# Kernel optimization log

Measured on AMD Instinct MI355X. Metric: run time of the kernel, lower is better.

## Reference

```python
import jax, jax.numpy as jnp
import numpy as np

B, L, DIM, H = 2, 2048, 2048, 16
D = DIM // H
EPS = 1e-6
CAP = 50.0
SCALE = D ** -0.5


def _rms_norm(x, w):
    # x: [B,H,L,D], normalize over last dim
    scale = jax.lax.rsqrt(jnp.maximum(jnp.mean(x * x, axis=-1, keepdims=True), EPS))
    return w * x * scale


def _rotate_half(x):
    x1, x2 = jnp.split(x, 2, axis=-1)
    return jnp.concatenate([-x2, x1], axis=-1)


def setup_inputs() -> dict:
    key = jax.random.key(0)
    ks = jax.random.split(key, 6)
    x = jax.random.normal(ks[0], (B, L, DIM), dtype=jnp.float32)
    w_qkv = jax.random.normal(ks[1], (3 * DIM, DIM), dtype=jnp.float32) * (DIM ** -0.5)
    w_out = jax.random.normal(ks[2], (DIM, DIM), dtype=jnp.float32) * (DIM ** -0.5)
    q_norm_w = jnp.ones((D,), dtype=jnp.float32)
    k_norm_w = jnp.ones((D,), dtype=jnp.float32)
    # rope tables [L, D]
    inv_freq = 1.0 / (10000.0 ** (np.arange(0, D, 2, dtype=np.float32) / D))
    t = np.arange(L, dtype=np.float32)
    freqs = np.outer(t, inv_freq)  # [L, D/2]
    emb = np.concatenate([freqs, freqs], axis=-1)  # [L, D]
    cos = jnp.asarray(np.cos(emb), dtype=jnp.float32)
    sin = jnp.asarray(np.sin(emb), dtype=jnp.float32)
    # additive causal mask [1,1,L,L]
    causal = np.triu(np.full((L, L), -1e9, dtype=np.float32), k=1)
    mask = jnp.asarray(causal)[None, None]
    return {"x": x, "w_qkv": w_qkv, "w_out": w_out, "q_norm_w": q_norm_w,
            "k_norm_w": k_norm_w, "cos": cos, "sin": sin, "mask": mask}


def reference(x, w_qkv, w_out, q_norm_w, k_norm_w, cos, sin, mask):
    b, l, _ = x.shape
    qkv = jnp.einsum('bld,ed->ble', x, w_qkv).reshape(b, l, 3, H, D)
    q, k, v = [jnp.transpose(qkv[:, :, i], (0, 2, 1, 3)) for i in range(3)]  # [B,H,L,D]
    q = _rms_norm(q, q_norm_w)
    k = _rms_norm(k, k_norm_w)
    # rope: cos/sin are [L,D] -> [1,1,L,D]
    c = cos[-l:, :][None, None]
    s = sin[-l:, :][None, None]
    q = q * c + _rotate_half(q) * s
    k = k * c + _rotate_half(k) * s
    attn = jnp.einsum('bhqd,bhkd->bhqk', q, k) * SCALE
    attn = jnp.tanh(attn / CAP) * CAP + mask
    probs = jax.nn.softmax(attn, axis=-1)
    o = jnp.einsum('bhqk,bhkd->bhqd', probs, v)
    o = jnp.transpose(o, (0, 2, 1, 3)).reshape(b, l, H * D)
    out = jnp.einsum('bld,ed->ble', o, w_out)
    return (out, (k, v))
```

## Files before the change

kernel.cpp:

```cpp
#include <hip/hip_runtime.h>
#include <hip/hip_bf16.h>
#include <stdint.h>

#define LL 2048
#define DD 128
#define HH 16

typedef float f32x4 __attribute__((ext_vector_type(4)));
typedef float f32x2 __attribute__((ext_vector_type(2)));
typedef short bf16x8 __attribute__((ext_vector_type(8)));
typedef short short4v __attribute__((ext_vector_type(4)));
typedef float float4v __attribute__((ext_vector_type(4)));

__device__ __forceinline__ float bf2f(short s) {
  union { unsigned u; float f; } v; v.u = ((unsigned)(unsigned short)s) << 16; return v.f;
}
__device__ __forceinline__ short f2bf(float f) {
  union { float f; unsigned u; } v; v.f = f;
  unsigned u = v.u;
  u += 0x7fffu + ((u >> 16) & 1u);
  return (short)(u >> 16);
}

__device__ __forceinline__ void gload_lds16(const void* g, void* lds) {
  __builtin_amdgcn_global_load_lds(
      (__attribute__((address_space(1))) unsigned int*)(void*)(uintptr_t)g,
      (__attribute__((address_space(3))) unsigned int*)lds, 16, 0, 0);
}

__global__ __launch_bounds__(256) void cast_all_kernel(
    const float* __restrict__ x, const float* __restrict__ wqkv,
    const float* __restrict__ wout, short* __restrict__ dst)
{
  long i4 = ((long)blockIdx.x * 256 + threadIdx.x) * 4;
  const float* src; long off;
  if (i4 < 8388608L)        { src = x;    off = i4; }
  else if (i4 < 20971520L)  { src = wqkv; off = i4 - 8388608L; }
  else                      { src = wout; off = i4 - 20971520L; }
  float4v v = *(const float4v*)(src + off);
  short4v o;
  o.x = f2bf(v.x); o.y = f2bf(v.y); o.z = f2bf(v.z); o.w = f2bf(v.w);
  *(short4v*)(dst + i4) = o;
}

template <typename OutT>
__global__ __launch_bounds__(256) void gemm_bt_kernel(
    const short* __restrict__ A, const short* __restrict__ Bm,
    OutT* __restrict__ C, int M, int N, int K)
{
  __shared__ __align__(16) short As[128 * 64];
  __shared__ __align__(16) short Bs[128 * 64];
  const int tid = threadIdx.x;
  const int lane = tid & 63;
  const int g = lane >> 4, j = lane & 15;
  const int m0 = blockIdx.y * 128, n0 = blockIdx.x * 128;
  const int wave = tid >> 6;
  const int wm = (wave >> 1) * 64, wn = (wave & 1) * 64;

  f32x4 acc[4][4];
  const f32x4 z = {0.f, 0.f, 0.f, 0.f};
#pragma unroll
  for (int i = 0; i < 4; ++i)
#pragma unroll
    for (int jj = 0; jj < 4; ++jj) acc[i][jj] = z;

  for (int k0 = 0; k0 < K; k0 += 64) {
#pragma unroll
    for (int it = 0; it < 4; ++it) {
      int c = it * 256 + tid;
      int row = c >> 3, ko = (c & 7) << 3;
      gload_lds16(A + (size_t)(m0 + row) * K + k0 + ko, As + c * 8);
    }
#pragma unroll
    for (int it = 0; it < 4; ++it) {
      int c = it * 256 + tid;
      int row = c >> 3, ko = (c & 7) << 3;
      gload_lds16(Bm + (size_t)(n0 + row) * K + k0 + ko, Bs + c * 8);
    }
    __syncthreads();
#pragma unroll
    for (int ks = 0; ks < 2; ++ks) {
      bf16x8 af[4], bfr[4];
#pragma unroll
      for (int i = 0; i < 4; ++i)
        af[i] = *(const bf16x8*)(As + (wm + i * 16 + j) * 64 + ks * 32 + g * 8);
#pragma unroll
      for (int i = 0; i < 4; ++i)
        bfr[i] = *(const bf16x8*)(Bs + (wn + i * 16 + j) * 64 + ks * 32 + g * 8);
#pragma unroll
      for (int i = 0; i < 4; ++i)
#pragma unroll
        for (int jj = 0; jj < 4; ++jj)
          acc[i][jj] = __builtin_amdgcn_mfma_f32_16x16x32_bf16(af[i], bfr[jj], acc[i][jj], 0, 0, 0);
    }
    __syncthreads();
  }
#pragma unroll
  for (int i = 0; i < 4; ++i)
#pragma unroll
    for (int jj = 0; jj < 4; ++jj)
#pragma unroll
      for (int r = 0; r < 4; ++r) {
        int row = m0 + wm + i * 16 + g * 4 + r;
        int col = n0 + wn + jj * 16 + j;
        if constexpr (sizeof(OutT) == 4)
          C[(size_t)row * N + col] = acc[i][jj][r];
        else
          C[(size_t)row * N + col] = f2bf(acc[i][jj][r]);
      }
}

__global__ __launch_bounds__(256) void normrope_kernel(
    const short* __restrict__ qkv, const float* __restrict__ qw,
    const float* __restrict__ kw, const float* __restrict__ cosb,
    const float* __restrict__ sinb, short* __restrict__ qo,
    float* __restrict__ ko, short* __restrict__ kb, float* __restrict__ vo)
{
  int wid = (blockIdx.x * 256 + threadIdx.x) >> 6;
  int lane = threadIdx.x & 63;
  int h = wid & 15;
  int rest = wid >> 4;
  int t = rest % 3;
  int bl = rest / 3;
  int l = bl & (LL - 1);
  int d0 = lane * 2;
  const short* src = qkv + (size_t)bl * 6144 + t * 2048 + h * 128 + d0;
  int raw = *(const int*)src;
  float v0 = bf2f((short)(raw & 0xffff));
  float v1 = bf2f((short)((raw >> 16) & 0xffff));
  size_t oidx = ((size_t)((bl >> 11) * HH + h) * LL + l) * DD + d0;
  if (t == 2) {
    f32x2 vv = {v0, v1};
    *(f32x2*)(vo + oidx) = vv;
    return;
  }
  float ss = v0 * v0 + v1 * v1;
#pragma unroll
  for (int m = 1; m <= 32; m <<= 1) ss += __shfl_xor(ss, m, 64);
  float scale = rsqrtf(fmaxf(ss * (1.0f / 128.0f), 1e-6f));
  const float* w = (t == 0) ? qw : kw;
  float n0 = w[d0] * v0 * scale;
  float n1 = w[d0 + 1] * v1 * scale;
  float c0 = cosb[l * 128 + d0], c1 = cosb[l * 128 + d0 + 1];
  float s0 = sinb[l * 128 + d0], s1 = sinb[l * 128 + d0 + 1];
  float p0 = __shfl_xor(n0, 32, 64);
  float p1 = __shfl_xor(n1, 32, 64);
  float r0 = (lane < 32) ? -p0 : p0;
  float r1 = (lane < 32) ? -p1 : p1;
  float o0 = n0 * c0 + r0 * s0;
  float o1 = n1 * c1 + r1 * s1;
  int pk = (int)((unsigned short)f2bf(o0) | ((unsigned)(unsigned short)f2bf(o1) << 16));
  if (t == 0) {
    *(int*)(qo + oidx) = pk;
  } else {
    f32x2 kk = {o0, o1};
    *(f32x2*)(ko + oidx) = kk;
    *(int*)(kb + oidx) = pk;
  }
}

__global__ __launch_bounds__(256) void transpose_v_kernel(
    const float* __restrict__ v, short* __restrict__ vT)
{
  __shared__ __align__(16) short tl[64 * 72];
  int bid = blockIdx.x;
  int dt = bid & 1;
  int lt = (bid >> 1) & 31;
  int bh = bid >> 6;
  int tid = threadIdx.x;
#pragma unroll
  for (int it = 0; it < 4; ++it) {
    int c = it * 256 + tid;
    int row = c >> 4, off = (c & 15) << 2;
    float4v val = *(const float4v*)(v + ((size_t)bh * LL + lt * 64 + row) * DD + dt * 64 + off);
    short4v s;
    s.x = f2bf(val.x); s.y = f2bf(val.y); s.z = f2bf(val.z); s.w = f2bf(val.w);
    *(short4v*)(tl + row * 72 + off) = s;
  }
  __syncthreads();
#pragma unroll
  for (int it = 0; it < 2; ++it) {
    int c = it * 256 + tid;
    int dr = c >> 3, lo = (c & 7) << 3;
    bf16x8 o;
#pragma unroll
    for (int i = 0; i < 8; ++i) o[i] = tl[(lo + i) * 72 + dr];
    *(bf16x8*)(vT + ((size_t)bh * DD + dt * 64 + dr) * LL + lt * 64 + lo) = o;
  }
}

__global__ __launch_bounds__(256, 2) void attn_kernel(
    const short* __restrict__ q, const short* __restrict__ k,
    const short* __restrict__ vT, short* __restrict__ o)
{
  __shared__ __align__(16) short Ks[64 * 136];
  __shared__ __align__(16) short Vs[128 * 72];
  __shared__ __align__(16) short Ps[128 * 72];
  int bid = blockIdx.x;
  int bh = bid & 31;
  int gq = (bid >> 5) & 7;
  int qt = (bid < 256) ? (15 - gq) : gq;
  int b = bh >> 4;
  int h = bh & 15;
  int tid = threadIdx.x;
  int lane = tid & 63;
  int w = tid >> 6;
  int g = lane >> 4, j = lane & 15;
  int q0 = qt * 128;
  int wrow = q0 + w * 32;

  bf16x8 qf[2][4];
#pragma unroll
  for (int mi = 0; mi < 2; ++mi)
#pragma unroll
    for (int ks = 0; ks < 4; ++ks)
      qf[mi][ks] = *(const bf16x8*)(q + ((size_t)bh * LL + wrow + mi * 16 + j) * DD + ks * 32 + g * 8);

  f32x4 accO[2][8];
  const f32x4 z = {0.f, 0.f, 0.f, 0.f};
#pragma unroll
  for (int mi = 0; mi < 2; ++mi)
#pragma unroll
    for (int n = 0; n < 8; ++n) accO[mi][n] = z;
  float lsum[2][4] = {{0.f,0.f,0.f,0.f},{0.f,0.f,0.f,0.f}};

  const float c2 = 0.0035355339059327379f;
  int ktmax = 2 * qt + 1;
  for (int kt = 0; kt <= ktmax; ++kt) {
    int k0 = kt * 64;
#pragma unroll
    for (int it = 0; it < 4; ++it) {
      int c = it * 256 + tid;
      int row = c >> 4, off = (c & 15) << 3;
      bf16x8 val = *(const bf16x8*)(k + ((size_t)bh * LL + k0 + row) * DD + off);
      *(bf16x8*)(Ks + row * 136 + off) = val;
    }
#pragma unroll
    for (int it = 0; it < 4; ++it) {
      int c = it * 256 + tid;
      int row = c >> 3, off = (c & 7) << 3;
      bf16x8 val = *(const bf16x8*)(vT + ((size_t)bh * DD + row) * LL + k0 + off);
      *(bf16x8*)(Vs + row * 72 + off) = val;
    }
    __syncthreads();

    f32x4 sa[2][4];
#pragma unroll
    for (int mi = 0; mi < 2; ++mi)
#pragma unroll
      for (int n = 0; n < 4; ++n) sa[mi][n] = z;
#pragma unroll
    for (int ks = 0; ks < 4; ++ks) {
#pragma unroll
      for (int n = 0; n < 4; ++n) {
        bf16x8 kf = *(const bf16x8*)(Ks + (n * 16 + j) * 136 + ks * 32 + g * 8);
#pragma unroll
        for (int mi = 0; mi < 2; ++mi)
          sa[mi][n] = __builtin_amdgcn_mfma_f32_16x16x32_bf16(qf[mi][ks], kf, sa[mi][n], 0, 0, 0);
      }
    }

#pragma unroll
    for (int mi = 0; mi < 2; ++mi) {
      const bool wmask = (k0 + 63) > (wrow + mi * 16);
#pragma unroll
      for (int r = 0; r < 4; ++r) {
        int row_g = wrow + mi * 16 + g * 4 + r;
#pragma unroll
        for (int n = 0; n < 4; ++n) {
          float e2 = __expf(sa[mi][n][r] * c2);
          float t = 38.f - 100.f * __builtin_amdgcn_rcpf(e2 + 1.f);
          float p = __expf(t);
          if (wmask && (k0 + n * 16 + j > row_g)) p = 0.f;
          lsum[mi][r] += p;
          Ps[(w * 32 + mi * 16 + g * 4 + r) * 72 + n * 16 + j] = f2bf(p);
        }
      }
    }
#pragma unroll
    for (int ks = 0; ks < 2; ++ks) {
      bf16x8 pf[2];
#pragma unroll
      for (int mi = 0; mi < 2; ++mi)
        pf[mi] = *(const bf16x8*)(Ps + (w * 32 + mi * 16 + j) * 72 + ks * 32 + g * 8);
#pragma unroll
      for (int n = 0; n < 8; ++n) {
        bf16x8 vf = *(const bf16x8*)(Vs + (n * 16 + j) * 72 + ks * 32 + g * 8);
#pragma unroll
        for (int mi = 0; mi < 2; ++mi)
          accO[mi][n] = __builtin_amdgcn_mfma_f32_16x16x32_bf16(pf[mi], vf, accO[mi][n], 0, 0, 0);
      }
    }
    __syncthreads();
  }

#pragma unroll
  for (int mi = 0; mi < 2; ++mi)
#pragma unroll
    for (int r = 0; r < 4; ++r) {
#pragma unroll
      for (int m = 1; m <= 8; m <<= 1) lsum[mi][r] += __shfl_xor(lsum[mi][r], m, 64);
    }

#pragma unroll
  for (int mi = 0; mi < 2; ++mi) {
    size_t obase = ((size_t)b * LL + wrow + mi * 16) * 2048 + h * 128;
#pragma unroll
    for (int r = 0; r < 4; ++r) {
      float inv = 1.f / lsum[mi][r];
#pragma unroll
      for (int n = 0; n < 8; ++n)
        o[obase + (size_t)(g * 4 + r) * 2048 + n * 16 + j] = f2bf(accO[mi][n][r] * inv);
    }
  }
}

extern "C" void kernel_launch(void* const* d_in, const int* in_sizes, int n_in,
                              void* d_out, int out_size, void* d_ws, size_t ws_size,
                              hipStream_t stream) {
  const float* x    = (const float*)d_in[0];
  const float* wqkv = (const float*)d_in[1];
  const float* wout = (const float*)d_in[2];
  const float* qw   = (const float*)d_in[3];
  const float* kw   = (const float*)d_in[4];
  const float* cosb = (const float*)d_in[5];
  const float* sinb = (const float*)d_in[6];

  float* out   = (float*)d_out;
  float* k_out = out + 8388608;
  float* v_out = out + 16777216;

  short* ws    = (short*)d_ws;
  short* xb    = ws;
  short* wqkvb = ws + 8388608;
  short* woutb = ws + 20971520;
  short* qkv   = ws + 25165824;
  short* qbuf  = xb;
  short* kbuf  = wqkvb;
  short* vT    = qkv;
  short* obuf  = qkv + 8388608;

  cast_all_kernel<<<24576, 256, 0, stream>>>(x, wqkv, wout, ws);
  gemm_bt_kernel<short><<<dim3(48, 32), 256, 0, stream>>>(xb, wqkvb, qkv, 4096, 6144, 2048);
  normrope_kernel<<<49152, 256, 0, stream>>>(qkv, qw, kw, cosb, sinb, qbuf, k_out, kbuf, v_out);
  transpose_v_kernel<<<2048, 256, 0, stream>>>(v_out, vT);
  attn_kernel<<<512, 256, 0, stream>>>(qbuf, kbuf, vT, obuf);
  gemm_bt_kernel<float><<<dim3(16, 32), 256, 0, stream>>>(obuf, woutb, out, 4096, 2048, 2048);
}
```

Before: 351.0 us.

## Replace QKV projection GEMM with 256x256 tile, 8-wave pipelined kernel

Adds a new GEMM for the QKV projection with 256x256 output tiles, 512 threads, and double-buffered LDS. Global loads go straight to LDS through global_load_lds with an XOR swizzle, and stages are interleaved with MFMA quarters under explicit barriers, vmcnt waits and setprio. The larger tile raises arithmetic intensity per LDS/global byte and overlaps loads with compute. The cost is more LDS (128KB), higher register pressure and a hand-scheduled pipeline with many barriers.

```diff
diff --git a/kernel.cpp b/kernel.cpp
--- a/kernel.cpp
+++ b/kernel.cpp
@@ -41,6 +41,126 @@
   short4v o;
   o.x = f2bf(v.x); o.y = f2bf(v.y); o.z = f2bf(v.z); o.w = f2bf(v.w);
   *(short4v*)(dst + i4) = o;
+}
+
+#define SCHED __builtin_amdgcn_sched_barrier(0)
+#define BARRIER { SCHED; __builtin_amdgcn_s_barrier(); SCHED; }
+
+#define STAGE(buf, opx, ptr, rb, ks, t)                                        \
+  { _Pragma("unroll") for (int l_ = 0; l_ < 2; ++l_) {                          \
+      int ch_ = l_ * 512 + tid;                                                 \
+      int row_ = ch_ >> 2, ci_ = ch_ & 3;                                       \
+      gload_lds16(ptr + (size_t)(rb + row_) * K + (t) * 64 + (ks) * 32 +        \
+                      ((ci_ ^ (row_ & 3)) << 3),                                \
+                  &lds[buf][opx][ks][ch_ << 3]);                                \
+  } }
+
+#define LDA(buf, mh, ks)                                                       \
+  { _Pragma("unroll") for (int mf_ = 0; mf_ < 4; ++mf_) {                       \
+      int r_ = wm * 128 + (mh) * 64 + mf_ * 16 + j;                             \
+      areg[mf_] = *(const bf16x8*)&lds[buf][0][ks][r_ * 32 + ((g ^ (j & 3)) << 3)]; \
+  } }
+
+#define LDB(dst, buf, ks)                                                      \
+  { _Pragma("unroll") for (int nf_ = 0; nf_ < 4; ++nf_) {                       \
+      int r_ = wn * 64 + nf_ * 16 + j;                                          \
+      dst[nf_] = *(const bf16x8*)&lds[buf][1][ks][r_ * 32 + ((g ^ (j & 3)) << 3)]; \
+  } }
+
+#define MFMAQ(mh, breg)                                                        \
+  { __builtin_amdgcn_s_setprio(1);                                             \
+    _Pragma("unroll") for (int mf_ = 0; mf_ < 4; ++mf_)                         \
+      _Pragma("unroll") for (int nf_ = 0; nf_ < 4; ++nf_)                       \
+        acc[(mh) * 4 + mf_][nf_] = __builtin_amdgcn_mfma_f32_16x16x32_bf16(     \
+            areg[mf_], breg[nf_], acc[(mh) * 4 + mf_][nf_], 0, 0, 0);           \
+    __builtin_amdgcn_s_setprio(0); }
+
+__global__ __launch_bounds__(512, 2) void gemm256_kernel(
+    const short* __restrict__ A, const short* __restrict__ Bm,
+    short* __restrict__ C, int M, int N, int K)
+{
+  __shared__ __align__(16) short lds[2][2][2][8192];
+  const int tid = threadIdx.x;
+  const int lane = tid & 63;
+  const int wid = tid >> 6;
+  const int wm = wid >> 2, wn = wid & 3;
+  const int g = lane >> 4, j = lane & 15;
+  const int m0 = blockIdx.y * 256, n0 = blockIdx.x * 256;
+  const int NT = K >> 6;
+
+  f32x4 acc[8][4];
+  const f32x4 z = {0.f, 0.f, 0.f, 0.f};
+#pragma unroll
+  for (int im = 0; im < 8; ++im)
+#pragma unroll
+    for (int nf = 0; nf < 4; ++nf) acc[im][nf] = z;
+
+  STAGE(0, 1, Bm, n0, 0, 0); STAGE(0, 1, Bm, n0, 1, 0);
+  STAGE(0, 0, A,  m0, 0, 0); STAGE(0, 0, A,  m0, 1, 0);
+  STAGE(1, 1, Bm, n0, 0, 1); STAGE(1, 1, Bm, n0, 1, 1);
+  STAGE(1, 0, A,  m0, 0, 1);
+  asm volatile("s_waitcnt vmcnt(6)" ::: "memory");
+  __builtin_amdgcn_s_barrier();
+  SCHED;
+
+  bf16x8 areg[4], b0r[4], b1r[4];
+#pragma unroll 1
+  for (int i = 0; i < (NT >> 1) - 1; ++i) {
+    int t0 = i * 2;
+    LDA(0, 0, 0); LDB(b0r, 0, 0);
+    STAGE(1, 0, A, m0, 1, t0 + 1);
+    BARRIER; MFMAQ(0, b0r); BARRIER;
+    LDA(0, 0, 1); LDB(b1r, 0, 1);
+    STAGE(0, 1, Bm, n0, 0, t0 + 2);
+    BARRIER; MFMAQ(0, b1r); BARRIER;
+    LDA(0, 1, 0);
+    STAGE(0, 1, Bm, n0, 1, t0 + 2);
+    BARRIER; MFMAQ(1, b0r); BARRIER;
+    LDA(0, 1, 1);
+    STAGE(0, 0, A, m0, 0, t0 + 2);
+    BARRIER; MFMAQ(1, b1r);
+    SCHED; asm volatile("s_waitcnt vmcnt(6)" ::: "memory");
+    __builtin_amdgcn_s_barrier(); SCHED;
+    LDA(1, 0, 0); LDB(b0r, 1, 0);
+    STAGE(0, 0, A, m0, 1, t0 + 2);
+    BARRIER; MFMAQ(0, b0r); BARRIER;
+    LDA(1, 0, 1); LDB(b1r, 1, 1);
+    STAGE(1, 1, Bm, n0, 0, t0 + 3);
+    BARRIER; MFMAQ(0, b1r); BARRIER;
+    LDA(1, 1, 0);
+    STAGE(1, 1, Bm, n0, 1, t0 + 3);
+    BARRIER; MFMAQ(1, b0r); BARRIER;
+    LDA(1, 1, 1);
+    STAGE(1, 0, A, m0, 0, t0 + 3);
+    BARRIER; MFMAQ(1, b1r);
+    SCHED; asm volatile("s_waitcnt vmcnt(6)" ::: "memory");
+    __builtin_amdgcn_s_barrier(); SCHED;
+  }
+  {
+    LDA(0, 0, 0); LDB(b0r, 0, 0);
+    STAGE(1, 0, A, m0, 1, NT - 1);
+    BARRIER; MFMAQ(0, b0r); BARRIER;
+    LDA(0, 0, 1); LDB(b1r, 0, 1);
+    BARRIER; MFMAQ(0, b1r); BARRIER;
+    LDA(0, 1, 0);
+    BARRIER; MFMAQ(1, b0r); BARRIER;
+    LDA(0, 1, 1);
+    BARRIER; MFMAQ(1, b1r);
+    SCHED; asm volatile("s_waitcnt vmcnt(0)" ::: "memory");
+    __builtin_amdgcn_s_barrier(); SCHED;
+    LDA(1, 0, 0); LDB(b0r, 1, 0); MFMAQ(0, b0r);
+    LDA(1, 0, 1); LDB(b1r, 1, 1); MFMAQ(0, b1r);
+    LDA(1, 1, 0); MFMAQ(1, b0r);
+    LDA(1, 1, 1); MFMAQ(1, b1r);
+  }
+#pragma unroll
+  for (int im = 0; im < 8; ++im)
+#pragma unroll
+    for (int nf = 0; nf < 4; ++nf)
+#pragma unroll
+      for (int r = 0; r < 4; ++r)
+        C[(size_t)(m0 + wm * 128 + im * 16 + g * 4 + r) * N + n0 + wn * 64 + nf * 16 + j] =
+            f2bf(acc[im][nf][r]);
 }
 
 template <typename OutT>
@@ -341,7 +461,7 @@
   short* obuf  = qkv + 8388608;
 
   cast_all_kernel<<<24576, 256, 0, stream>>>(x, wqkv, wout, ws);
-  gemm_bt_kernel<short><<<dim3(48, 32), 256, 0, stream>>>(xb, wqkvb, qkv, 4096, 6144, 2048);
+  gemm256_kernel<<<dim3(24, 16), 512, 0, stream>>>(xb, wqkvb, qkv, 4096, 6144, 2048);
   normrope_kernel<<<49152, 256, 0, stream>>>(qkv, qw, kw, cosb, sinb, qbuf, k_out, kbuf, v_out);
   transpose_v_kernel<<<2048, 256, 0, stream>>>(v_out, vT);
   attn_kernel<<<512, 256, 0, stream>>>(qbuf, kbuf, vT, obuf);
```

Result: faster. 320.8 us (-8.6%).

## Replace QKV projection GEMM with 256x256 double-buffered pipelined MFMA kernel

Applied to the files above, without the earlier changes.

Adds a new 512-thread GEMM kernel that computes 256x256 output tiles and is used for the QKV projection. It double-buffers LDS with direct global-to-LDS loads, uses XOR-swizzled LDS layouts, and interleaves LDS fragment reads with MFMA issue under explicit waitcnt, barrier and priority control. The aim is more data reuse per tile and better overlap of memory and compute than the old 128x128 kernel. The loop hardcodes K=2048 (32 k-tiles) and tile-multiple dimensions, and the larger register and LDS footprint may limit occupancy.

```diff
diff --git a/kernel.cpp b/kernel.cpp
--- a/kernel.cpp
+++ b/kernel.cpp
@@ -41,6 +41,111 @@
   short4v o;
   o.x = f2bf(v.x); o.y = f2bf(v.y); o.z = f2bf(v.z); o.w = f2bf(v.w);
   *(short4v*)(dst + i4) = o;
+}
+
+#define SCHED __builtin_amdgcn_sched_barrier(0)
+#define BARRIER { SCHED; __builtin_amdgcn_s_barrier(); SCHED; }
+#define LGKM(n) { asm volatile("s_waitcnt lgkmcnt(" #n ")" ::: "memory"); SCHED; }
+#define VMC(n)  { asm volatile("s_waitcnt vmcnt(" #n ")" ::: "memory"); SCHED; }
+
+#define STAGE(buf, opx, ptr, rb, ks, t)                                        \
+  { _Pragma("unroll") for (int l_ = 0; l_ < 2; ++l_) {                          \
+      int ch_ = l_ * 512 + tid;                                                 \
+      int row_ = ch_ >> 2, ci_ = ch_ & 3;                                       \
+      gload_lds16(ptr + (size_t)(rb + row_) * K + (t) * 64 + (ks) * 32 +        \
+                      ((ci_ ^ ((row_ >> 1) & 3)) << 3),                         \
+                  &lds[buf][opx][ks][ch_ << 3]);                                \
+  } }
+
+#define STAGE_TILE(buf, t)                                                     \
+  { STAGE(buf, 0, A,  m0, 0, t); STAGE(buf, 0, A,  m0, 1, t);                   \
+    STAGE(buf, 1, Bm, n0, 0, t); STAGE(buf, 1, Bm, n0, 1, t); }
+
+#define LDA_TO(dst, buf, mh)                                                   \
+  { _Pragma("unroll") for (int ks_ = 0; ks_ < 2; ++ks_)                         \
+    _Pragma("unroll") for (int mf_ = 0; mf_ < 4; ++mf_) {                       \
+      int r_ = wm * 128 + (mh) * 64 + mf_ * 16 + j;                             \
+      dst[ks_][mf_] = *(const bf16x8*)&lds[buf][0][ks_][r_ * 32 + ((g ^ ((j >> 1) & 3)) << 3)]; \
+  } }
+
+#define LDB_TO(dst, buf)                                                       \
+  { _Pragma("unroll") for (int ks_ = 0; ks_ < 2; ++ks_)                         \
+    _Pragma("unroll") for (int nf_ = 0; nf_ < 4; ++nf_) {                       \
+      int r_ = wn * 64 + nf_ * 16 + j;                                          \
+      dst[ks_][nf_] = *(const bf16x8*)&lds[buf][1][ks_][r_ * 32 + ((g ^ ((j >> 1) & 3)) << 3)]; \
+  } }
+
+#define MFMA32(asrc, mh)                                                       \
+  { __builtin_amdgcn_s_setprio(1);                                             \
+    _Pragma("unroll") for (int ks_ = 0; ks_ < 2; ++ks_)                         \
+      _Pragma("unroll") for (int mf_ = 0; mf_ < 4; ++mf_)                       \
+        _Pragma("unroll") for (int nf_ = 0; nf_ < 4; ++nf_)                     \
+          acc[(mh) * 4 + mf_][nf_] = __builtin_amdgcn_mfma_f32_16x16x32_bf16(   \
+              asrc[ks_][mf_], bb[ks_][nf_], acc[(mh) * 4 + mf_][nf_], 0, 0, 0); \
+    __builtin_amdgcn_s_setprio(0); }
+
+#define TILE_BODY(B, t, DO_STAGE, DO_PF, VKIND)                                \
+  {                                                                            \
+    LDB_TO(bb, B);                                                             \
+    LDA_TO(aB, B, 1);                                                          \
+    LGKM(8);                               \
+    MFMA32(aA, 0);                                         \
+    LGKM(0);                                                                   \
+    BARRIER;                                 \
+    if (DO_STAGE) { STAGE_TILE(B, (t) + 2); }                                  \
+    if ((VKIND) == 8) { VMC(8); }                                              \
+    else if ((VKIND) == 0) { VMC(0); }                                         \
+    BARRIER;                                 \
+    if (DO_PF) { LDA_TO(aA, (B) ^ 1, 0); SCHED; }         \
+    MFMA32(aB, 1);                                                             \
+  }
+
+__global__ __launch_bounds__(512, 2) void gemm256_kernel(
+    const short* __restrict__ A, const short* __restrict__ Bm,
+    short* __restrict__ C, int M, int N, int K)
+{
+  __shared__ __align__(16) short lds[2][2][2][8192];
+  const int tid = threadIdx.x;
+  const int lane = tid & 63;
+  const int wid = tid >> 6;
+  const int wm = wid >> 2, wn = wid & 3;
+  const int g = lane >> 4, j = lane & 15;
+  const int m0 = blockIdx.y * 256, n0 = blockIdx.x * 256;
+
+  f32x4 acc[8][4];
+  const f32x4 z = {0.f, 0.f, 0.f, 0.f};
+#pragma unroll
+  for (int im = 0; im < 8; ++im)
+#pragma unroll
+    for (int nf = 0; nf < 4; ++nf) acc[im][nf] = z;
+
+  bf16x8 aA[2][4], aB[2][4], bb[2][4];
+
+  STAGE_TILE(0, 0);
+  STAGE_TILE(1, 1);
+  VMC(8);
+  __builtin_amdgcn_s_barrier(); SCHED;
+  LDA_TO(aA, 0, 0);
+
+#pragma unroll 1
+  for (int i = 0; i < 14; ++i) {
+    int t0 = i * 2;
+    TILE_BODY(0, t0,     1, 1, 8);
+    TILE_BODY(1, t0 + 1, 1, 1, 8);
+  }
+  TILE_BODY(0, 28, 1, 1, 8);
+  TILE_BODY(1, 29, 1, 1, 8);
+  TILE_BODY(0, 30, 0, 1, 0);
+  TILE_BODY(1, 31, 0, 0, 2);
+
+#pragma unroll
+  for (int im = 0; im < 8; ++im)
+#pragma unroll
+    for (int nf = 0; nf < 4; ++nf)
+#pragma unroll
+      for (int r = 0; r < 4; ++r)
+        C[(size_t)(m0 + wm * 128 + im * 16 + g * 4 + r) * N + n0 + wn * 64 + nf * 16 + j] =
+            f2bf(acc[im][nf][r]);
 }
 
 template <typename OutT>
@@ -341,7 +446,7 @@
   short* obuf  = qkv + 8388608;
 
   cast_all_kernel<<<24576, 256, 0, stream>>>(x, wqkv, wout, ws);
-  gemm_bt_kernel<short><<<dim3(48, 32), 256, 0, stream>>>(xb, wqkvb, qkv, 4096, 6144, 2048);
+  gemm256_kernel<<<dim3(24, 16), 512, 0, stream>>>(xb, wqkvb, qkv, 4096, 6144, 2048);
   normrope_kernel<<<49152, 256, 0, stream>>>(qkv, qw, kw, cosb, sinb, qbuf, k_out, kbuf, v_out);
   transpose_v_kernel<<<2048, 256, 0, stream>>>(v_out, vT);
   attn_kernel<<<512, 256, 0, stream>>>(qbuf, kbuf, vT, obuf);
```

Result: no change. 344.7 us (-1.8%).

## Pipeline GEMMs with double-buffered swizzled LDS and swizzle attention K/V tiles

Applied to the files above, without the earlier changes.

Replaces the 128x128 single-buffered GEMM with a 128x256, 512-thread kernel. It double-buffers K-slices in LDS with XOR-swizzled layout, explicit vmcnt waits and priority hints, so global loads overlap MFMA work and LDS bank conflicts drop. The attention kernel swaps padded K/V shared tiles for XOR-swizzled unpadded ones and raises wave priority around its MFMA blocks. The GEMM loop is hardcoded for K=2048 (32 tiles of 64), and the larger block lowers the number of blocks per GEMM launch.

```diff
diff --git a/kernel.cpp b/kernel.cpp
--- a/kernel.cpp
+++ b/kernel.cpp
@@ -43,70 +43,111 @@
   *(short4v*)(dst + i4) = o;
 }
 
+#define SCHED __builtin_amdgcn_sched_barrier(0)
+
+#define STAGE_A(buf, ks, t)                                                    \
+  { int row_ = tid >> 2, ci_ = tid & 3;                                         \
+    gload_lds16(A + (size_t)(m0 + row_) * K + (t) * 64 + (ks) * 32 +            \
+                    ((ci_ ^ ((row_ >> 1) & 3)) << 3),                           \
+                ldsA[buf][ks] + tid * 8); }
+
+#define STAGE_B(buf, ks, t)                                                    \
+  { _Pragma("unroll") for (int l_ = 0; l_ < 2; ++l_) {                          \
+      int ch_ = l_ * 512 + tid;                                                 \
+      int row_ = ch_ >> 2, ci_ = ch_ & 3;                                       \
+      gload_lds16(Bm + (size_t)(n0 + row_) * K + (t) * 64 + (ks) * 32 +         \
+                      ((ci_ ^ ((row_ >> 1) & 3)) << 3),                         \
+                  ldsB[buf][ks] + ch_ * 8); } }
+
+#define LDA2(buf, ks)                                                          \
+  { _Pragma("unroll") for (int mf_ = 0; mf_ < 4; ++mf_) {                       \
+      int r_ = wm * 64 + mf_ * 16 + j;                                          \
+      areg[mf_] = *(const bf16x8*)&ldsA[buf][ks][r_ * 32 + ((g ^ ((j >> 1) & 3)) << 3)]; } }
+
+#define LDB2(buf, ks)                                                          \
+  { _Pragma("unroll") for (int nf_ = 0; nf_ < 4; ++nf_) {                       \
+      int r_ = wn * 64 + nf_ * 16 + j;                                          \
+      breg[nf_] = *(const bf16x8*)&ldsB[buf][ks][r_ * 32 + ((g ^ ((j >> 1) & 3)) << 3)]; } }
+
+#define MFMA16                                                                 \
+  { __builtin_amdgcn_s_setprio(1);                                             \
+    _Pragma("unroll") for (int mf_ = 0; mf_ < 4; ++mf_)                         \
+      _Pragma("unroll") for (int nf_ = 0; nf_ < 4; ++nf_)                       \
+        acc[mf_][nf_] = __builtin_amdgcn_mfma_f32_16x16x32_bf16(                \
+            areg[mf_], breg[nf_], acc[mf_][nf_], 0, 0, 0);                      \
+    __builtin_amdgcn_s_setprio(0); }
+
+#define PH_S(RB, KS, SB, SKS, ST)                                              \
+  LDA2(RB, KS); LDB2(RB, KS);                                                   \
+  STAGE_A(SB, SKS, ST); STAGE_B(SB, SKS, ST);                                   \
+  __builtin_amdgcn_s_barrier();                                                 \
+  MFMA16;                                                                       \
+  asm volatile("s_waitcnt vmcnt(6)" ::: "memory");                              \
+  __builtin_amdgcn_s_barrier();
+
+#define PH_N(RB, KS, VKSTR)                                                    \
+  LDA2(RB, KS); LDB2(RB, KS);                                                   \
+  __builtin_amdgcn_s_barrier();                                                 \
+  MFMA16;                                                                       \
+  asm volatile("s_waitcnt " VKSTR ::: "memory");                                \
+  __builtin_amdgcn_s_barrier();
+
 template <typename OutT>
-__global__ __launch_bounds__(256) void gemm_bt_kernel(
+__global__ __launch_bounds__(512, 1) void gemm128x256_kernel(
     const short* __restrict__ A, const short* __restrict__ Bm,
     OutT* __restrict__ C, int M, int N, int K)
 {
-  __shared__ __align__(16) short As[128 * 64];
-  __shared__ __align__(16) short Bs[128 * 64];
+  __shared__ __align__(16) short ldsA[2][2][4096];
+  __shared__ __align__(16) short ldsB[2][2][8192];
   const int tid = threadIdx.x;
   const int lane = tid & 63;
+  const int wid = tid >> 6;
+  const int wm = wid >> 2, wn = wid & 3;
   const int g = lane >> 4, j = lane & 15;
-  const int m0 = blockIdx.y * 128, n0 = blockIdx.x * 128;
-  const int wave = tid >> 6;
-  const int wm = (wave >> 1) * 64, wn = (wave & 1) * 64;
+  const int m0 = blockIdx.y * 128, n0 = blockIdx.x * 256;
 
   f32x4 acc[4][4];
   const f32x4 z = {0.f, 0.f, 0.f, 0.f};
 #pragma unroll
-  for (int i = 0; i < 4; ++i)
-#pragma unroll
-    for (int jj = 0; jj < 4; ++jj) acc[i][jj] = z;
-
-  for (int k0 = 0; k0 < K; k0 += 64) {
-#pragma unroll
-    for (int it = 0; it < 4; ++it) {
-      int c = it * 256 + tid;
-      int row = c >> 3, ko = (c & 7) << 3;
-      gload_lds16(A + (size_t)(m0 + row) * K + k0 + ko, As + c * 8);
-    }
-#pragma unroll
-    for (int it = 0; it < 4; ++it) {
-      int c = it * 256 + tid;
-      int row = c >> 3, ko = (c & 7) << 3;
-      gload_lds16(Bm + (size_t)(n0 + row) * K + k0 + ko, Bs + c * 8);
-    }
-    __syncthreads();
-#pragma unroll
-    for (int ks = 0; ks < 2; ++ks) {
-      bf16x8 af[4], bfr[4];
-#pragma unroll
-      for (int i = 0; i < 4; ++i)
-        af[i] = *(const bf16x8*)(As + (wm + i * 16 + j) * 64 + ks * 32 + g * 8);
-#pragma unroll
-      for (int i = 0; i < 4; ++i)
-        bfr[i] = *(const bf16x8*)(Bs + (wn + i * 16 + j) * 64 + ks * 32 + g * 8);
-#pragma unroll
-      for (int i = 0; i < 4; ++i)
-#pragma unroll
-        for (int jj = 0; jj < 4; ++jj)
-          acc[i][jj] = __builtin_amdgcn_mfma_f32_16x16x32_bf16(af[i], bfr[jj], acc[i][jj], 0, 0, 0);
-    }
-    __syncthreads();
-  }
-#pragma unroll
-  for (int i = 0; i < 4; ++i)
-#pragma unroll
-    for (int jj = 0; jj < 4; ++jj)
+  for (int mf = 0; mf < 4; ++mf)
+#pragma unroll
+    for (int nf = 0; nf < 4; ++nf) acc[mf][nf] = z;
+
+  bf16x8 areg[4], breg[4];
+
+  STAGE_A(0, 0, 0); STAGE_B(0, 0, 0);
+  STAGE_A(0, 1, 0); STAGE_B(0, 1, 0);
+  STAGE_A(1, 0, 1); STAGE_B(1, 0, 1);
+  asm volatile("s_waitcnt vmcnt(6)" ::: "memory");
+  __builtin_amdgcn_s_barrier();
+  SCHED;
+
+#pragma unroll 1
+  for (int i = 0; i < 15; ++i) {
+    int t0 = 2 * i;
+    PH_S(0, 0, 1, 1, t0 + 1);
+    PH_S(0, 1, 0, 0, t0 + 2);
+    PH_S(1, 0, 0, 1, t0 + 2);
+    PH_S(1, 1, 1, 0, t0 + 3);
+  }
+  PH_S(0, 0, 1, 1, 31);
+  PH_N(0, 1, "vmcnt(3)");
+  PH_N(1, 0, "vmcnt(0)");
+  LDA2(1, 1); LDB2(1, 1);
+  MFMA16;
+
+#pragma unroll
+  for (int mf = 0; mf < 4; ++mf)
+#pragma unroll
+    for (int nf = 0; nf < 4; ++nf)
 #pragma unroll
       for (int r = 0; r < 4; ++r) {
-        int row = m0 + wm + i * 16 + g * 4 + r;
-        int col = n0 + wn + jj * 16 + j;
+        int row = m0 + wm * 64 + mf * 16 + g * 4 + r;
+        int col = n0 + wn * 64 + nf * 16 + j;
         if constexpr (sizeof(OutT) == 4)
-          C[(size_t)row * N + col] = acc[i][jj][r];
+          C[(size_t)row * N + col] = acc[mf][nf][r];
         else
-          C[(size_t)row * N + col] = f2bf(acc[i][jj][r]);
+          C[(size_t)row * N + col] = f2bf(acc[mf][nf][r]);
       }
 }
 
@@ -193,8 +234,8 @@
     const short* __restrict__ q, const short* __restrict__ k,
     const short* __restrict__ vT, short* __restrict__ o)
 {
-  __shared__ __align__(16) short Ks[64 * 136];
-  __shared__ __align__(16) short Vs[128 * 72];
+  __shared__ __align__(16) short Ks[64 * 128];
+  __shared__ __align__(16) short Vs[128 * 64];
   __shared__ __align__(16) short Ps[128 * 72];
   int bid = blockIdx.x;
   int bh = bid & 31;
@@ -233,14 +274,14 @@
       int c = it * 256 + tid;
       int row = c >> 4, off = (c & 15) << 3;
       bf16x8 val = *(const bf16x8*)(k + ((size_t)bh * LL + k0 + row) * DD + off);
-      *(bf16x8*)(Ks + row * 136 + off) = val;
+      *(bf16x8*)(Ks + row * 128 + (off ^ ((row & 7) << 3))) = val;
     }
 #pragma unroll
     for (int it = 0; it < 4; ++it) {
       int c = it * 256 + tid;
       int row = c >> 3, off = (c & 7) << 3;
       bf16x8 val = *(const bf16x8*)(vT + ((size_t)bh * DD + row) * LL + k0 + off);
-      *(bf16x8*)(Vs + row * 72 + off) = val;
+      *(bf16x8*)(Vs + row * 64 + (off ^ ((row & 7) << 3))) = val;
     }
     __syncthreads();
 
@@ -249,16 +290,18 @@
     for (int mi = 0; mi < 2; ++mi)
 #pragma unroll
       for (int n = 0; n < 4; ++n) sa[mi][n] = z;
+    __builtin_amdgcn_s_setprio(1);
 #pragma unroll
     for (int ks = 0; ks < 4; ++ks) {
 #pragma unroll
       for (int n = 0; n < 4; ++n) {
-        bf16x8 kf = *(const bf16x8*)(Ks + (n * 16 + j) * 136 + ks * 32 + g * 8);
+        bf16x8 kf = *(const bf16x8*)(Ks + (n * 16 + j) * 128 + ((ks * 32 + g * 8) ^ ((j & 7) << 3)));
 #pragma unroll
         for (int mi = 0; mi < 2; ++mi)
           sa[mi][n] = __builtin_amdgcn_mfma_f32_16x16x32_bf16(qf[mi][ks], kf, sa[mi][n], 0, 0, 0);
       }
     }
+    __builtin_amdgcn_s_setprio(0);
 
 #pragma unroll
     for (int mi = 0; mi < 2; ++mi) {
@@ -277,6 +320,7 @@
         }
       }
     }
+    __builtin_amdgcn_s_setprio(1);
 #pragma unroll
     for (int ks = 0; ks < 2; ++ks) {
       bf16x8 pf[2];
@@ -285,12 +329,13 @@
         pf[mi] = *(const bf16x8*)(Ps + (w * 32 + mi * 16 + j) * 72 + ks * 32 + g * 8);
 #pragma unroll
       for (int n = 0; n < 8; ++n) {
-        bf16x8 vf = *(const bf16x8*)(Vs + (n * 16 + j) * 72 + ks * 32 + g * 8);
+        bf16x8 vf = *(const bf16x8*)(Vs + (n * 16 + j) * 64 + ((ks * 32 + g * 8) ^ ((j & 7) << 3)));
 #pragma unroll
         for (int mi = 0; mi < 2; ++mi)
           accO[mi][n] = __builtin_amdgcn_mfma_f32_16x16x32_bf16(pf[mi], vf, accO[mi][n], 0, 0, 0);
       }
     }
+    __builtin_amdgcn_s_setprio(0);
     __syncthreads();
   }
 
@@ -341,9 +386,9 @@
   short* obuf  = qkv + 8388608;
 
   cast_all_kernel<<<24576, 256, 0, stream>>>(x, wqkv, wout, ws);
-  gemm_bt_kernel<short><<<dim3(48, 32), 256, 0, stream>>>(xb, wqkvb, qkv, 4096, 6144, 2048);
+  gemm128x256_kernel<short><<<dim3(24, 32), 512, 0, stream>>>(xb, wqkvb, qkv, 4096, 6144, 2048);
   normrope_kernel<<<49152, 256, 0, stream>>>(qkv, qw, kw, cosb, sinb, qbuf, k_out, kbuf, v_out);
   transpose_v_kernel<<<2048, 256, 0, stream>>>(v_out, vT);
   attn_kernel<<<512, 256, 0, stream>>>(qbuf, kbuf, vT, obuf);
-  gemm_bt_kernel<float><<<dim3(16, 32), 256, 0, stream>>>(obuf, woutb, out, 4096, 2048, 2048);
-}
+  gemm128x256_kernel<float><<<dim3(8, 32), 512, 0, stream>>>(obuf, woutb, out, 4096, 2048, 2048);
+}
```

Result: faster. 333.1 us (-5.1%).
